# Kernel optimization log

Measured on AMD Instinct MI355X. Metric: run time of the kernel, lower is better.

The kernel has to match this reference:

```python
import jax, jax.numpy as jnp
import numpy as np

D_MODEL, H, D_FF = 1024, 16, 4096
B, S = 2, 2048
EPS = 1e-05


def layer_norm(x, gamma, beta):
    # Matches torch: mean and UNBIASED std over last dim, scalar gamma/beta,
    # and eps added to std (not variance).
    mean = jnp.mean(x, axis=-1, keepdims=True)
    var = jnp.sum((x - mean) ** 2, axis=-1, keepdims=True) / (x.shape[-1] - 1)
    return gamma * (x - mean) / (jnp.sqrt(var) + EPS) + beta


def setup_inputs() -> dict:
    key = jax.random.key(0)
    ks = jax.random.split(key, 16)
    sd = 1.0 / np.sqrt(D_MODEL)
    sf = 1.0 / np.sqrt(D_FF)
    return {
        "x": jax.random.normal(ks[0], (B, S, D_MODEL), jnp.float32),
        "mask": jnp.ones((1, 1, S, S), jnp.int32),
        "wq": jax.random.uniform(ks[1], (D_MODEL, D_MODEL), jnp.float32, -sd, sd),
        "bq": jax.random.uniform(ks[2], (D_MODEL,), jnp.float32, -sd, sd),
        "wk": jax.random.uniform(ks[3], (D_MODEL, D_MODEL), jnp.float32, -sd, sd),
        "bk": jax.random.uniform(ks[4], (D_MODEL,), jnp.float32, -sd, sd),
        "wv": jax.random.uniform(ks[5], (D_MODEL, D_MODEL), jnp.float32, -sd, sd),
        "bv": jax.random.uniform(ks[6], (D_MODEL,), jnp.float32, -sd, sd),
        "wo": jax.random.uniform(ks[7], (D_MODEL, D_MODEL), jnp.float32, -sd, sd),
        "bo": jax.random.uniform(ks[8], (D_MODEL,), jnp.float32, -sd, sd),
        "w1": jax.random.uniform(ks[9], (D_FF, D_MODEL), jnp.float32, -sd, sd),
        "b1": jax.random.uniform(ks[10], (D_FF,), jnp.float32, -sd, sd),
        "w2": jax.random.uniform(ks[11], (D_MODEL, D_FF), jnp.float32, -sf, sf),
        "b2": jax.random.uniform(ks[12], (D_MODEL,), jnp.float32, -sf, sf),
        "gamma1": jnp.ones((1,), jnp.float32),
        "beta1": jnp.zeros((1,), jnp.float32),
        "gamma2": jnp.ones((1,), jnp.float32),
        "beta2": jnp.zeros((1,), jnp.float32),
    }


def reference(x, mask, wq, bq, wk, bk, wv, bv, wo, bo, w1, b1, w2, b2,
              gamma1, beta1, gamma2, beta2):
    d_k = D_MODEL // H

    # --- residual 1: pre-LN self-attention ---
    xn = layer_norm(x, gamma1, beta1)
    q = (xn @ wq.T + bq).reshape(B, S, H, d_k).transpose(0, 2, 1, 3)
    k = (xn @ wk.T + bk).reshape(B, S, H, d_k).transpose(0, 2, 1, 3)
    v = (xn @ wv.T + bv).reshape(B, S, H, d_k).transpose(0, 2, 1, 3)

    scores = jnp.einsum("bhqd,bhkd->bhqk", q, k) / jnp.sqrt(
        jnp.asarray(d_k, x.dtype))
    scores = jnp.where(mask == 0, jnp.asarray(-1e9, x.dtype), scores)
    attn = jax.nn.softmax(scores, axis=-1)
    ctx = jnp.einsum("bhqk,bhkd->bhqd", attn, v)
    ctx = ctx.transpose(0, 2, 1, 3).reshape(B, S, D_MODEL)
    x = x + (ctx @ wo.T + bo)

    # --- residual 2: pre-LN feed-forward ---
    xn = layer_norm(x, gamma2, beta2)
    h = jax.nn.relu(xn @ w1.T + b1)
    x = x + (h @ w2.T + b2)
    return x
```

## Files before the change

kernel.cpp:

```cpp
#include <hip/hip_runtime.h>


typedef __bf16 bf16_t;
typedef __attribute__((ext_vector_type(8))) __bf16 bf16x8;
typedef __attribute__((ext_vector_type(4))) __bf16 bf16x4;
typedef __attribute__((ext_vector_type(4))) float f32x4;

#define MB (1024ull * 1024ull)
#define QSCALE 0.18033688011112043f

__device__ __forceinline__ void gload_lds16(const bf16_t* g, bf16_t* l) {
    __builtin_amdgcn_global_load_lds(
        (const __attribute__((address_space(1))) void*)g,
        (__attribute__((address_space(3))) void*)l, 16, 0, 0);
}

__device__ __forceinline__ int swz(int row, int col) {
    return row * 64 + ((((col >> 3) ^ row) & 7) << 3) + (col & 7);
}

__global__ __launch_bounds__(256) void cvt_kernel(const float* __restrict__ in,
                                                  bf16_t* __restrict__ out, int n4) {
    int i = blockIdx.x * 256 + threadIdx.x;
    if (i < n4) {
        float4 v = ((const float4*)in)[i];
        bf16x4 o = {(__bf16)v.x, (__bf16)v.y, (__bf16)v.z, (__bf16)v.w};
        ((bf16x4*)out)[i] = o;
    }
}

__global__ __launch_bounds__(256) void ln_kernel(const float* __restrict__ x,
                                                 bf16_t* __restrict__ out,
                                                 const float* __restrict__ gamma,
                                                 const float* __restrict__ beta) {
    const int lane = threadIdx.x & 63;
    const int row = blockIdx.x * 4 + (threadIdx.x >> 6);
    const float* xr = x + (size_t)row * 1024;
    float4 v[4];
    float s = 0.f;
#pragma unroll
    for (int i = 0; i < 4; ++i) {
        v[i] = ((const float4*)xr)[i * 64 + lane];
        s += v[i].x + v[i].y + v[i].z + v[i].w;
    }
#pragma unroll
    for (int o = 32; o; o >>= 1) s += __shfl_xor(s, o);
    float mean = s * (1.f / 1024.f);
    float vs = 0.f;
#pragma unroll
    for (int i = 0; i < 4; ++i) {
        float a = v[i].x - mean, b = v[i].y - mean, c = v[i].z - mean, d = v[i].w - mean;
        vs += a * a + b * b + c * c + d * d;
    }
#pragma unroll
    for (int o = 32; o; o >>= 1) vs += __shfl_xor(vs, o);
    float inv = 1.f / (sqrtf(vs * (1.f / 1023.f)) + 1e-5f);
    float g = gamma[0] * inv, bb = beta[0];
    bf16_t* orow = out + (size_t)row * 1024;
#pragma unroll
    for (int i = 0; i < 4; ++i) {
        bf16x4 ov = {(__bf16)((v[i].x - mean) * g + bb), (__bf16)((v[i].y - mean) * g + bb),
                     (__bf16)((v[i].z - mean) * g + bb), (__bf16)((v[i].w - mean) * g + bb)};
        *(bf16x4*)(orow + (i * 64 + lane) * 4) = ov;
    }
}

template <int KERN>
__global__ __launch_bounds__(512, 2) void gemm256(
    const bf16_t* __restrict__ A, const bf16_t* __restrict__ Bw, int K,
    const float* __restrict__ bias0, const float* __restrict__ bias1,
    const float* __restrict__ bias2, void* __restrict__ o0, void* __restrict__ o1,
    void* __restrict__ o2) {
    __shared__ bf16_t L[4 * 16384];
    const int t = threadIdx.x, lane = t & 63, w = t >> 6;
    const int wm = w >> 2, wn = w & 3;
    const int l15 = lane & 15, l4 = lane >> 4;
    const int bm = blockIdx.x, bn = blockIdx.y;
    const int NT = K >> 5;
    const bf16_t* Ab = A + (size_t)bm * 256 * K;
    const bf16_t* Bb = Bw + (size_t)bn * 256 * K;
    const int srow = t >> 2, pcol = (t & 3) * 8;
    f32x4 acc[8][4] = {};

    auto stageA = [&](int tt) {
        bf16_t* s = L + (tt & 3) * 16384;
        const int kb = tt * 32;
#pragma unroll
        for (int i = 0; i < 2; ++i) {
            int row = i * 128 + srow;
            int lcol = pcol ^ ((row & 3) << 3);
            gload_lds16(Ab + (size_t)row * K + kb + lcol, s + i * 4096 + t * 8);
        }
    };
    auto stageB = [&](int tt) {
        bf16_t* s = L + (tt & 3) * 16384 + 8192;
        const int kb = tt * 32;
#pragma unroll
        for (int i = 0; i < 2; ++i) {
            int row = i * 128 + srow;
            int lcol = pcol ^ ((row & 3) << 3);
            gload_lds16(Bb + (size_t)row * K + kb + lcol, s + i * 4096 + t * 8);
        }
    };

    stageA(0); stageB(0); stageA(1); stageB(1); stageA(2); stageB(2);
    asm volatile("s_waitcnt vmcnt(8)" ::: "memory");
    __builtin_amdgcn_s_barrier();

    for (int tt = 0; tt < NT; ++tt) {
        bf16_t* s = L + (tt & 3) * 16384;
        bf16_t* sB = s + 8192;
        bf16x8 af[4], bfr[4];
#pragma unroll
        for (int m = 0; m < 4; ++m) {
            int row = wm * 128 + m * 16 + l15;
            af[m] = *(const bf16x8*)(s + row * 32 + ((l4 * 8) ^ ((row & 3) << 3)));
        }
#pragma unroll
        for (int n = 0; n < 4; ++n) {
            int row = wn * 64 + n * 16 + l15;
            bfr[n] = *(const bf16x8*)(sB + row * 32 + ((l4 * 8) ^ ((row & 3) << 3)));
        }
        if (tt + 3 < NT) stageA(tt + 3);
        __builtin_amdgcn_s_barrier();
        __builtin_amdgcn_s_setprio(1);
#pragma unroll
        for (int m = 0; m < 4; ++m)
#pragma unroll
            for (int n = 0; n < 4; ++n)
                acc[m][n] = __builtin_amdgcn_mfma_f32_16x16x32_bf16(af[m], bfr[n], acc[m][n],
                                                                   0, 0, 0);
        __builtin_amdgcn_s_setprio(0);
        __builtin_amdgcn_s_barrier();
#pragma unroll
        for (int m = 0; m < 4; ++m) {
            int row = wm * 128 + 64 + m * 16 + l15;
            af[m] = *(const bf16x8*)(s + row * 32 + ((l4 * 8) ^ ((row & 3) << 3)));
        }
        if (tt + 3 < NT) stageB(tt + 3);
        __builtin_amdgcn_s_barrier();
        __builtin_amdgcn_s_setprio(1);
#pragma unroll
        for (int m = 0; m < 4; ++m)
#pragma unroll
            for (int n = 0; n < 4; ++n)
                acc[4 + m][n] = __builtin_amdgcn_mfma_f32_16x16x32_bf16(af[m], bfr[n],
                                                                       acc[4 + m][n], 0, 0, 0);
        __builtin_amdgcn_s_setprio(0);
        if (tt + 3 < NT)
            asm volatile("s_waitcnt vmcnt(8)" ::: "memory");
        else if (tt + 2 < NT)
            asm volatile("s_waitcnt vmcnt(4)" ::: "memory");
        else
            asm volatile("s_waitcnt vmcnt(0)" ::: "memory");
        __builtin_amdgcn_s_barrier();
    }

    if (KERN == 1) {
        const int colb = bn * 256 + wn * 64;
        float bb[4];
#pragma unroll
        for (int n = 0; n < 4; ++n) bb[n] = bias0[colb + n * 16 + l15];
#pragma unroll
        for (int m = 0; m < 8; ++m) {
            const int row0 = bm * 256 + wm * 128 + m * 16 + (l4 << 2);
#pragma unroll
            for (int n = 0; n < 4; ++n)
#pragma unroll
                for (int j = 0; j < 4; ++j) {
                    float v = acc[m][n][j] + bb[n];
                    ((bf16_t*)o0)[(size_t)(row0 + j) * 4096 + colb + n * 16 + l15] =
                        (bf16_t)(v > 0.f ? v : 0.f);
                }
        }
        return;
    }
    if (bn < 8) {
        const bool isq = bn < 4;
        const float* bias = isq ? bias0 : bias1;
        const int head = (bn & 3) * 4 + wn;
        const int b = (bm * 256) >> 11;
        const int srow0 = (bm * 256 + wm * 128) & 2047;
        bf16_t* dst = (bf16_t*)(isq ? o0 : o1) + ((size_t)(b * 16 + head) << 17);
        float bb[4];
#pragma unroll
        for (int n = 0; n < 4; ++n) bb[n] = bias[head * 64 + n * 16 + l15];
#pragma unroll
        for (int m = 0; m < 8; ++m)
#pragma unroll
            for (int n = 0; n < 4; ++n)
#pragma unroll
                for (int j = 0; j < 4; ++j) {
                    int srw = srow0 + m * 16 + (l4 << 2) + j;
                    float v = acc[m][n][j] + bb[n];
                    if (isq) v *= QSCALE;
                    dst[((size_t)srw << 6) + n * 16 + l15] = (bf16_t)v;
                }
    } else {
        const int head = (bn - 8) * 4 + wn;
        const int b = (bm * 256) >> 11;
        const int sbase = (bm * 256 + wm * 128) & 2047;
        bf16_t* P = L + w * 8192;
        float bb[4];
#pragma unroll
        for (int n = 0; n < 4; ++n) bb[n] = bias2[head * 64 + n * 16 + l15];
#pragma unroll
        for (int m = 0; m < 8; ++m)
#pragma unroll
            for (int n = 0; n < 4; ++n) {
                int d = n * 16 + l15;
                int sl = m * 16 + (l4 << 2);
                bf16x4 pk = {(__bf16)(acc[m][n][0] + bb[n]), (__bf16)(acc[m][n][1] + bb[n]),
                             (__bf16)(acc[m][n][2] + bb[n]), (__bf16)(acc[m][n][3] + bb[n])};
                *(bf16x4*)(P + d * 128 + (sl ^ ((d & 7) << 3))) = pk;
            }
#pragma unroll
        for (int p = 0; p < 16; ++p) {
            int id = p * 64 + lane;
            int d = id >> 4, c8 = (id & 15) * 8;
            bf16x8 vv = *(const bf16x8*)(P + d * 128 + (c8 ^ ((d & 7) << 3)));
            *(bf16x8*)((bf16_t*)o2 + (((size_t)(b * 16 + head) * 64 + d) << 11) + sbase + c8) =
                vv;
        }
    }
}

__global__ __launch_bounds__(256, 2) void gemm128p(
    const bf16_t* __restrict__ A, const bf16_t* __restrict__ Bw, int K,
    const float* __restrict__ bias, const float* __restrict__ resid,
    float* __restrict__ out) {
    __shared__ bf16_t L[4 * 6144];
    const int t = threadIdx.x, lane = t & 63, w = t >> 6;
    const int wr = w >> 1, wc = w & 1;
    const int l15 = lane & 15, l4 = lane >> 4;
    const int bm = blockIdx.x, bn = blockIdx.y;
    const int NT = K >> 5;
    const bf16_t* Ab = A + (size_t)bm * 64 * K;
    const bf16_t* Bb = Bw + (size_t)bn * 128 * K;
    const int srow = t >> 2, pcol = (t & 3) * 8;
    f32x4 acc[2][4] = {};

    auto STAGE = [&](int tt) {
        bf16_t* s = L + (tt & 3) * 6144;
        const int kb = tt * 32;
        {
            int lcol = pcol ^ ((srow & 3) << 3);
            gload_lds16(Ab + (size_t)srow * K + kb + lcol, s + t * 8);
        }
#pragma unroll
        for (int i = 0; i < 2; ++i) {
            int row = i * 64 + srow;
            int lcol = pcol ^ ((row & 3) << 3);
            gload_lds16(Bb + (size_t)row * K + kb + lcol, s + 2048 + i * 2048 + t * 8);
        }
    };

    STAGE(0); STAGE(1); STAGE(2);
    asm volatile("s_waitcnt vmcnt(6)" ::: "memory");
    __builtin_amdgcn_s_barrier();

    for (int tt = 0; tt < NT; ++tt) {
        bf16_t* s = L + (tt & 3) * 6144;
        bf16x8 af[2], bfr[4];
#pragma unroll
        for (int m = 0; m < 2; ++m) {
            int row = wr * 32 + m * 16 + l15;
            af[m] = *(const bf16x8*)(s + row * 32 + ((l4 * 8) ^ ((row & 3) << 3)));
        }
#pragma unroll
        for (int n = 0; n < 4; ++n) {
            int row = wc * 64 + n * 16 + l15;
            bfr[n] = *(const bf16x8*)(s + 2048 + row * 32 + ((l4 * 8) ^ ((row & 3) << 3)));
        }
        if (tt + 3 < NT) STAGE(tt + 3);
        __builtin_amdgcn_s_barrier();
        __builtin_amdgcn_s_setprio(1);
#pragma unroll
        for (int m = 0; m < 2; ++m)
#pragma unroll
            for (int n = 0; n < 4; ++n)
                acc[m][n] = __builtin_amdgcn_mfma_f32_16x16x32_bf16(af[m], bfr[n], acc[m][n],
                                                                   0, 0, 0);
        __builtin_amdgcn_s_setprio(0);
        if (tt + 3 < NT)
            asm volatile("s_waitcnt vmcnt(6)" ::: "memory");
        else if (tt + 2 < NT)
            asm volatile("s_waitcnt vmcnt(3)" ::: "memory");
        else
            asm volatile("s_waitcnt vmcnt(0)" ::: "memory");
        __builtin_amdgcn_s_barrier();
    }

#pragma unroll
    for (int m = 0; m < 2; ++m) {
        const int row0 = bm * 64 + wr * 32 + m * 16 + (l4 << 2);
#pragma unroll
        for (int n = 0; n < 4; ++n) {
            const int col = bn * 128 + wc * 64 + n * 16 + l15;
#pragma unroll
            for (int j = 0; j < 4; ++j) {
                const int row = row0 + j;
                out[(size_t)row * 1024 + col] =
                    resid[(size_t)row * 1024 + col] + acc[m][n][j] + bias[col];
            }
        }
    }
}

__global__ __launch_bounds__(256) void attn_kernel(const bf16_t* __restrict__ q,
                                                   const bf16_t* __restrict__ k,
                                                   const bf16_t* __restrict__ vt,
                                                   bf16_t* __restrict__ ctx) {
    __shared__ bf16_t Kl[64 * 64];
    __shared__ bf16_t Vl[64 * 64];
    __shared__ bf16_t Pl[4][16 * 64];
    const int t = threadIdx.x, lane = t & 63, w = t >> 6;
    const int qt0 = blockIdx.x * 64;
    const int bh = blockIdx.y;
    const bf16_t* qg = q + (size_t)bh * 2048 * 64;
    const bf16_t* kg = k + (size_t)bh * 2048 * 64;
    const bf16_t* vg = vt + (size_t)bh * 64 * 2048;
    const int r = t >> 3, c8 = (t & 7) * 8;
    const int l15 = lane & 15, l4 = lane >> 4;

    *(bf16x8*)(Kl + swz(r, c8)) = *(const bf16x8*)(qg + (size_t)(qt0 + r) * 64 + c8);
    *(bf16x8*)(Kl + swz(r + 32, c8)) = *(const bf16x8*)(qg + (size_t)(qt0 + r + 32) * 64 + c8);
    __syncthreads();
    bf16x8 qf[2];
    qf[0] = *(const bf16x8*)(Kl + swz(w * 16 + l15, l4 * 8));
    qf[1] = *(const bf16x8*)(Kl + swz(w * 16 + l15, 32 + l4 * 8));
    __syncthreads();

    f32x4 o[4] = {};
    float mi = -1e30f, li = 0.f;

    {
        bf16x8 k0 = *(const bf16x8*)(kg + (size_t)r * 64 + c8);
        bf16x8 k1 = *(const bf16x8*)(kg + (size_t)(r + 32) * 64 + c8);
        bf16x8 v0 = *(const bf16x8*)(vg + (size_t)r * 2048 + c8);
        bf16x8 v1 = *(const bf16x8*)(vg + (size_t)(r + 32) * 2048 + c8);
        *(bf16x8*)(Kl + swz(r, c8)) = k0;
        *(bf16x8*)(Kl + swz(r + 32, c8)) = k1;
        *(bf16x8*)(Vl + swz(r, c8)) = v0;
        *(bf16x8*)(Vl + swz(r + 32, c8)) = v1;
    }

    for (int kt = 0; kt < 2048; kt += 64) {
        __syncthreads();
        bf16x8 k0, k1, v0, v1;
        const bool more = (kt + 64) < 2048;
        if (more) {
            k0 = *(const bf16x8*)(kg + (size_t)(kt + 64 + r) * 64 + c8);
            k1 = *(const bf16x8*)(kg + (size_t)(kt + 64 + r + 32) * 64 + c8);
            v0 = *(const bf16x8*)(vg + (size_t)r * 2048 + kt + 64 + c8);
            v1 = *(const bf16x8*)(vg + (size_t)(r + 32) * 2048 + kt + 64 + c8);
        }
        f32x4 sT[4] = {};
        __builtin_amdgcn_s_setprio(1);
#pragma unroll
        for (int kk = 0; kk < 2; ++kk) {
            bf16x8 kf[4];
#pragma unroll
            for (int n = 0; n < 4; ++n)
                kf[n] = *(const bf16x8*)(Kl + swz(n * 16 + l15, kk * 32 + l4 * 8));
#pragma unroll
            for (int n = 0; n < 4; ++n)
                sT[n] = __builtin_amdgcn_mfma_f32_16x16x32_bf16(kf[n], qf[kk], sT[n], 0, 0, 0);
        }
        __builtin_amdgcn_s_setprio(0);
        float mx = fmaxf(fmaxf(sT[0][0], sT[0][1]), fmaxf(sT[0][2], sT[0][3]));
#pragma unroll
        for (int n = 1; n < 4; ++n)
            mx = fmaxf(mx, fmaxf(fmaxf(sT[n][0], sT[n][1]), fmaxf(sT[n][2], sT[n][3])));
        mx = fmaxf(mx, __shfl_xor(mx, 16));
        mx = fmaxf(mx, __shfl_xor(mx, 32));
        if (!__all(mx <= mi + 8.f)) {
            float mn = fmaxf(mi, mx);
            float al = exp2f(mi - mn);
            mi = mn;
            li *= al;
#pragma unroll
            for (int jr = 0; jr < 4; ++jr) {
                float alo = __shfl(al, (lane & 0x30) | (l4 * 4 + jr));
#pragma unroll
                for (int n = 0; n < 4; ++n) o[n][jr] *= alo;
            }
        }
        float rs = 0.f;
#pragma unroll
        for (int n = 0; n < 4; ++n) {
            float p0 = exp2f(sT[n][0] - mi);
            float p1 = exp2f(sT[n][1] - mi);
            float p2 = exp2f(sT[n][2] - mi);
            float p3 = exp2f(sT[n][3] - mi);
            rs += (p0 + p1) + (p2 + p3);
            bf16x4 pk = {(__bf16)p0, (__bf16)p1, (__bf16)p2, (__bf16)p3};
            *(bf16x4*)(&Pl[w][swz(l15, n * 16 + (l4 << 2))]) = pk;
        }
        rs += __shfl_xor(rs, 16);
        rs += __shfl_xor(rs, 32);
        li += rs;
        __builtin_amdgcn_s_setprio(1);
#pragma unroll
        for (int kk = 0; kk < 2; ++kk) {
            bf16x8 pa = *(const bf16x8*)(&Pl[w][swz(l15, kk * 32 + l4 * 8)]);
            bf16x8 vb[4];
#pragma unroll
            for (int n = 0; n < 4; ++n)
                vb[n] = *(const bf16x8*)(Vl + swz(n * 16 + l15, kk * 32 + l4 * 8));
#pragma unroll
            for (int n = 0; n < 4; ++n)
                o[n] = __builtin_amdgcn_mfma_f32_16x16x32_bf16(pa, vb[n], o[n], 0, 0, 0);
        }
        __builtin_amdgcn_s_setprio(0);
        __syncthreads();
        if (more) {
            *(bf16x8*)(Kl + swz(r, c8)) = k0;
            *(bf16x8*)(Kl + swz(r + 32, c8)) = k1;
            *(bf16x8*)(Vl + swz(r, c8)) = v0;
            *(bf16x8*)(Vl + swz(r + 32, c8)) = v1;
        }
    }
#pragma unroll
    for (int jr = 0; jr < 4; ++jr) {
        float inv = 1.f / __shfl(li, (lane & 0x30) | (l4 * 4 + jr));
        int row = qt0 + w * 16 + l4 * 4 + jr;
        size_t base = ((size_t)(bh >> 4) * 2048 + row) * 1024 + (bh & 15) * 64;
#pragma unroll
        for (int n = 0; n < 4; ++n)
            ctx[base + n * 16 + l15] = (bf16_t)(o[n][jr] * inv);
    }
}

extern "C" void kernel_launch(void* const* d_in, const int* in_sizes, int n_in,
                              void* d_out, int out_size, void* d_ws, size_t ws_size,
                              hipStream_t stream) {
    const float* x = (const float*)d_in[0];
    const float* wq = (const float*)d_in[2];
    const float* bq = (const float*)d_in[3];
    const float* wk = (const float*)d_in[4];
    const float* bk = (const float*)d_in[5];
    const float* wv = (const float*)d_in[6];
    const float* bv = (const float*)d_in[7];
    const float* wo = (const float*)d_in[8];
    const float* bo = (const float*)d_in[9];
    const float* w1 = (const float*)d_in[10];
    const float* b1 = (const float*)d_in[11];
    const float* w2 = (const float*)d_in[12];
    const float* b2 = (const float*)d_in[13];
    const float* gamma1 = (const float*)d_in[14];
    const float* beta1 = (const float*)d_in[15];
    const float* gamma2 = (const float*)d_in[16];
    const float* beta2 = (const float*)d_in[17];

    char* ws = (char*)d_ws;
    bf16_t* wqkv = (bf16_t*)(ws + 0);
    bf16_t* wob = (bf16_t*)(ws + 6 * MB);
    bf16_t* w1b = (bf16_t*)(ws + 8 * MB);
    bf16_t* w2b = (bf16_t*)(ws + 16 * MB);
    bf16_t* xnb = (bf16_t*)(ws + 24 * MB);
    bf16_t* qb = (bf16_t*)(ws + 32 * MB);
    bf16_t* kb = (bf16_t*)(ws + 40 * MB);
    bf16_t* vtb = (bf16_t*)(ws + 48 * MB);
    bf16_t* ctxb = (bf16_t*)(ws + 56 * MB);
    float* x1 = (float*)(ws + 64 * MB);
    bf16_t* hb = (bf16_t*)(ws + 32 * MB);

    cvt_kernel<<<1024, 256, 0, stream>>>(wq, wqkv, 262144);
    cvt_kernel<<<1024, 256, 0, stream>>>(wk, wqkv + 1024 * 1024, 262144);
    cvt_kernel<<<1024, 256, 0, stream>>>(wv, wqkv + 2 * 1024 * 1024, 262144);
    cvt_kernel<<<1024, 256, 0, stream>>>(wo, wob, 262144);
    cvt_kernel<<<4096, 256, 0, stream>>>(w1, w1b, 1048576);
    cvt_kernel<<<4096, 256, 0, stream>>>(w2, w2b, 1048576);

    ln_kernel<<<1024, 256, 0, stream>>>(x, xnb, gamma1, beta1);
    gemm256<0><<<dim3(16, 12), 512, 0, stream>>>(xnb, wqkv, 1024, bq, bk, bv, qb, kb, vtb);
    attn_kernel<<<dim3(32, 32), 256, 0, stream>>>(qb, kb, vtb, ctxb);
    gemm128p<<<dim3(64, 8), 256, 0, stream>>>(ctxb, wob, 1024, bo, x, x1);
    ln_kernel<<<1024, 256, 0, stream>>>(x1, xnb, gamma2, beta2);
    gemm256<1><<<dim3(16, 16), 512, 0, stream>>>(xnb, w1b, 1024, b1, nullptr, nullptr, hb,
                                                 nullptr, nullptr);
    gemm128p<<<dim3(64, 8), 256, 0, stream>>>(hb, w2b, 4096, b2, x1, (float*)d_out);
}
```

Baseline: 260.0 us.

## Rewrite attention with 32x32x16 MFMA and register-resident P via permlane swap

The attention kernel now gives each wave 32 query rows and uses 32x32x16 bf16 MFMAs. Q fragments load straight from global memory, and the softmax probabilities are repacked in registers with permlane32_swap instead of a round-trip through LDS. This halves the grid, doubles K/V reuse per block, drops the per-row alpha shuffles and uses the hardware exp2. The six weight-conversion launches are merged into a single kernel to cut launch overhead. The trade-off is higher register pressure (launch_bounds 256,2) and fewer blocks for the attention grid.

```diff
diff --git a/kernel.cpp b/kernel.cpp
--- a/kernel.cpp
+++ b/kernel.cpp
@@ -4,7 +4,11 @@
 typedef __bf16 bf16_t;
 typedef __attribute__((ext_vector_type(8))) __bf16 bf16x8;
 typedef __attribute__((ext_vector_type(4))) __bf16 bf16x4;
+typedef __attribute__((ext_vector_type(2))) __bf16 bf16x2;
 typedef __attribute__((ext_vector_type(4))) float f32x4;
+typedef __attribute__((ext_vector_type(16))) float f32x16;
+typedef __attribute__((ext_vector_type(2))) unsigned uint32x2;
+typedef __attribute__((ext_vector_type(4))) unsigned uint32x4;
 
 #define MB (1024ull * 1024ull)
 #define QSCALE 0.18033688011112043f
@@ -19,14 +23,30 @@
     return row * 64 + ((((col >> 3) ^ row) & 7) << 3) + (col & 7);
 }
 
-__global__ __launch_bounds__(256) void cvt_kernel(const float* __restrict__ in,
-                                                  bf16_t* __restrict__ out, int n4) {
-    int i = blockIdx.x * 256 + threadIdx.x;
-    if (i < n4) {
-        float4 v = ((const float4*)in)[i];
-        bf16x4 o = {(__bf16)v.x, (__bf16)v.y, (__bf16)v.z, (__bf16)v.w};
-        ((bf16x4*)out)[i] = o;
-    }
+__device__ __forceinline__ unsigned cvtpk(float a, float b) {
+    bf16x2 v = {(__bf16)a, (__bf16)b};
+    return __builtin_bit_cast(unsigned, v);
+}
+
+__global__ __launch_bounds__(256) void cvt_all(
+    const float* __restrict__ wq, const float* __restrict__ wk,
+    const float* __restrict__ wv, const float* __restrict__ wo,
+    const float* __restrict__ w1, const float* __restrict__ w2,
+    bf16_t* __restrict__ wqkv, bf16_t* __restrict__ wob, bf16_t* __restrict__ w1b,
+    bf16_t* __restrict__ w2b) {
+    const int b = blockIdx.x, t = threadIdx.x;
+    const float* in;
+    bf16_t* out;
+    int i;
+    if (b < 1024) { in = wq; out = wqkv; i = b * 256 + t; }
+    else if (b < 2048) { in = wk; out = wqkv + 1048576; i = (b - 1024) * 256 + t; }
+    else if (b < 3072) { in = wv; out = wqkv + 2097152; i = (b - 2048) * 256 + t; }
+    else if (b < 4096) { in = wo; out = wob; i = (b - 3072) * 256 + t; }
+    else if (b < 8192) { in = w1; out = w1b; i = (b - 4096) * 256 + t; }
+    else { in = w2; out = w2b; i = (b - 8192) * 256 + t; }
+    float4 v = ((const float4*)in)[i];
+    bf16x4 o = {(__bf16)v.x, (__bf16)v.y, (__bf16)v.z, (__bf16)v.w};
+    ((bf16x4*)out)[i] = o;
 }
 
 __global__ __launch_bounds__(256) void ln_kernel(const float* __restrict__ x,
@@ -307,31 +327,27 @@
     }
 }
 
-__global__ __launch_bounds__(256) void attn_kernel(const bf16_t* __restrict__ q,
-                                                   const bf16_t* __restrict__ k,
-                                                   const bf16_t* __restrict__ vt,
-                                                   bf16_t* __restrict__ ctx) {
+__global__ __launch_bounds__(256, 2) void attn_kernel(const bf16_t* __restrict__ q,
+                                                      const bf16_t* __restrict__ k,
+                                                      const bf16_t* __restrict__ vt,
+                                                      bf16_t* __restrict__ ctx) {
     __shared__ bf16_t Kl[64 * 64];
     __shared__ bf16_t Vl[64 * 64];
-    __shared__ bf16_t Pl[4][16 * 64];
     const int t = threadIdx.x, lane = t & 63, w = t >> 6;
-    const int qt0 = blockIdx.x * 64;
     const int bh = blockIdx.y;
     const bf16_t* qg = q + (size_t)bh * 2048 * 64;
     const bf16_t* kg = k + (size_t)bh * 2048 * 64;
     const bf16_t* vg = vt + (size_t)bh * 64 * 2048;
     const int r = t >> 3, c8 = (t & 7) * 8;
-    const int l15 = lane & 15, l4 = lane >> 4;
-
-    *(bf16x8*)(Kl + swz(r, c8)) = *(const bf16x8*)(qg + (size_t)(qt0 + r) * 64 + c8);
-    *(bf16x8*)(Kl + swz(r + 32, c8)) = *(const bf16x8*)(qg + (size_t)(qt0 + r + 32) * 64 + c8);
-    __syncthreads();
-    bf16x8 qf[2];
-    qf[0] = *(const bf16x8*)(Kl + swz(w * 16 + l15, l4 * 8));
-    qf[1] = *(const bf16x8*)(Kl + swz(w * 16 + l15, 32 + l4 * 8));
-    __syncthreads();
-
-    f32x4 o[4] = {};
+    const int l31 = lane & 31, h = lane >> 5;
+    const int qrow = blockIdx.x * 128 + w * 32 + l31;
+
+    bf16x8 qf[4];
+#pragma unroll
+    for (int kd = 0; kd < 4; ++kd)
+        qf[kd] = *(const bf16x8*)(qg + (size_t)qrow * 64 + kd * 16 + h * 8);
+
+    f32x16 o0 = {}, o1 = {};
     float mi = -1e30f, li = 0.f;
 
     {
@@ -355,62 +371,66 @@
             v0 = *(const bf16x8*)(vg + (size_t)r * 2048 + kt + 64 + c8);
             v1 = *(const bf16x8*)(vg + (size_t)(r + 32) * 2048 + kt + 64 + c8);
         }
-        f32x4 sT[4] = {};
+        f32x16 sT0 = {}, sT1 = {};
         __builtin_amdgcn_s_setprio(1);
 #pragma unroll
-        for (int kk = 0; kk < 2; ++kk) {
-            bf16x8 kf[4];
-#pragma unroll
-            for (int n = 0; n < 4; ++n)
-                kf[n] = *(const bf16x8*)(Kl + swz(n * 16 + l15, kk * 32 + l4 * 8));
-#pragma unroll
-            for (int n = 0; n < 4; ++n)
-                sT[n] = __builtin_amdgcn_mfma_f32_16x16x32_bf16(kf[n], qf[kk], sT[n], 0, 0, 0);
+        for (int kd = 0; kd < 4; ++kd) {
+            bf16x8 ka0 = *(const bf16x8*)(Kl + swz(l31, kd * 16 + h * 8));
+            bf16x8 ka1 = *(const bf16x8*)(Kl + swz(32 + l31, kd * 16 + h * 8));
+            sT0 = __builtin_amdgcn_mfma_f32_32x32x16_bf16(ka0, qf[kd], sT0, 0, 0, 0);
+            sT1 = __builtin_amdgcn_mfma_f32_32x32x16_bf16(ka1, qf[kd], sT1, 0, 0, 0);
         }
         __builtin_amdgcn_s_setprio(0);
-        float mx = fmaxf(fmaxf(sT[0][0], sT[0][1]), fmaxf(sT[0][2], sT[0][3]));
-#pragma unroll
-        for (int n = 1; n < 4; ++n)
-            mx = fmaxf(mx, fmaxf(fmaxf(sT[n][0], sT[n][1]), fmaxf(sT[n][2], sT[n][3])));
-        mx = fmaxf(mx, __shfl_xor(mx, 16));
+        float mx = fmaxf(sT0[0], sT0[1]);
+#pragma unroll
+        for (int i = 2; i < 16; ++i) mx = fmaxf(mx, sT0[i]);
+#pragma unroll
+        for (int i = 0; i < 16; ++i) mx = fmaxf(mx, sT1[i]);
         mx = fmaxf(mx, __shfl_xor(mx, 32));
         if (!__all(mx <= mi + 8.f)) {
             float mn = fmaxf(mi, mx);
-            float al = exp2f(mi - mn);
+            float al = __builtin_amdgcn_exp2f(mi - mn);
             mi = mn;
             li *= al;
-#pragma unroll
-            for (int jr = 0; jr < 4; ++jr) {
-                float alo = __shfl(al, (lane & 0x30) | (l4 * 4 + jr));
-#pragma unroll
-                for (int n = 0; n < 4; ++n) o[n][jr] *= alo;
-            }
-        }
+            o0 *= al;
+            o1 *= al;
+        }
+        f32x16 e0, e1;
         float rs = 0.f;
 #pragma unroll
-        for (int n = 0; n < 4; ++n) {
-            float p0 = exp2f(sT[n][0] - mi);
-            float p1 = exp2f(sT[n][1] - mi);
-            float p2 = exp2f(sT[n][2] - mi);
-            float p3 = exp2f(sT[n][3] - mi);
-            rs += (p0 + p1) + (p2 + p3);
-            bf16x4 pk = {(__bf16)p0, (__bf16)p1, (__bf16)p2, (__bf16)p3};
-            *(bf16x4*)(&Pl[w][swz(l15, n * 16 + (l4 << 2))]) = pk;
-        }
-        rs += __shfl_xor(rs, 16);
+        for (int i = 0; i < 16; ++i) {
+            e0[i] = __builtin_amdgcn_exp2f(sT0[i] - mi);
+            rs += e0[i];
+        }
+#pragma unroll
+        for (int i = 0; i < 16; ++i) {
+            e1[i] = __builtin_amdgcn_exp2f(sT1[i] - mi);
+            rs += e1[i];
+        }
         rs += __shfl_xor(rs, 32);
         li += rs;
+        bf16x8 pa[4];
+#pragma unroll
+        for (int kd = 0; kd < 4; ++kd) {
+            const f32x16& e = (kd < 2) ? e0 : e1;
+            const int R0l = 8 * (kd & 1);
+            const int R0h = R0l + 4;
+            unsigned U0 = cvtpk(e[R0l + 0], e[R0l + 1]);
+            unsigned V0 = cvtpk(e[R0l + 2], e[R0l + 3]);
+            unsigned U1 = cvtpk(e[R0h + 0], e[R0h + 1]);
+            unsigned V1 = cvtpk(e[R0h + 2], e[R0h + 3]);
+            uint32x2 ru = __builtin_amdgcn_permlane32_swap(U0, U1, false, false);
+            uint32x2 rv = __builtin_amdgcn_permlane32_swap(V0, V1, false, false);
+            uint32x4 pw = {ru.x, rv.x, ru.y, rv.y};
+            pa[kd] = __builtin_bit_cast(bf16x8, pw);
+        }
         __builtin_amdgcn_s_setprio(1);
 #pragma unroll
-        for (int kk = 0; kk < 2; ++kk) {
-            bf16x8 pa = *(const bf16x8*)(&Pl[w][swz(l15, kk * 32 + l4 * 8)]);
-            bf16x8 vb[4];
-#pragma unroll
-            for (int n = 0; n < 4; ++n)
-                vb[n] = *(const bf16x8*)(Vl + swz(n * 16 + l15, kk * 32 + l4 * 8));
-#pragma unroll
-            for (int n = 0; n < 4; ++n)
-                o[n] = __builtin_amdgcn_mfma_f32_16x16x32_bf16(pa, vb[n], o[n], 0, 0, 0);
+        for (int kd = 0; kd < 4; ++kd) {
+            bf16x8 va0 = *(const bf16x8*)(Vl + swz(l31, kd * 16 + h * 8));
+            bf16x8 va1 = *(const bf16x8*)(Vl + swz(32 + l31, kd * 16 + h * 8));
+            o0 = __builtin_amdgcn_mfma_f32_32x32x16_bf16(va0, pa[kd], o0, 0, 0, 0);
+            o1 = __builtin_amdgcn_mfma_f32_32x32x16_bf16(va1, pa[kd], o1, 0, 0, 0);
         }
         __builtin_amdgcn_s_setprio(0);
         __syncthreads();
@@ -421,14 +441,16 @@
             *(bf16x8*)(Vl + swz(r + 32, c8)) = v1;
         }
     }
-#pragma unroll
-    for (int jr = 0; jr < 4; ++jr) {
-        float inv = 1.f / __shfl(li, (lane & 0x30) | (l4 * 4 + jr));
-        int row = qt0 + w * 16 + l4 * 4 + jr;
-        size_t base = ((size_t)(bh >> 4) * 2048 + row) * 1024 + (bh & 15) * 64;
-#pragma unroll
-        for (int n = 0; n < 4; ++n)
-            ctx[base + n * 16 + l15] = (bf16_t)(o[n][jr] * inv);
+    float inv = 1.f / li;
+    size_t base = ((size_t)(bh >> 4) * 2048 + qrow) * 1024 + (bh & 15) * 64;
+#pragma unroll
+    for (int g = 0; g < 4; ++g) {
+        bf16x4 ov0 = {(__bf16)(o0[4 * g + 0] * inv), (__bf16)(o0[4 * g + 1] * inv),
+                      (__bf16)(o0[4 * g + 2] * inv), (__bf16)(o0[4 * g + 3] * inv)};
+        *(bf16x4*)(ctx + base + 8 * g + 4 * h) = ov0;
+        bf16x4 ov1 = {(__bf16)(o1[4 * g + 0] * inv), (__bf16)(o1[4 * g + 1] * inv),
+                      (__bf16)(o1[4 * g + 2] * inv), (__bf16)(o1[4 * g + 3] * inv)};
+        *(bf16x4*)(ctx + base + 32 + 8 * g + 4 * h) = ov1;
     }
 }
 
@@ -466,16 +488,11 @@
     float* x1 = (float*)(ws + 64 * MB);
     bf16_t* hb = (bf16_t*)(ws + 32 * MB);
 
-    cvt_kernel<<<1024, 256, 0, stream>>>(wq, wqkv, 262144);
-    cvt_kernel<<<1024, 256, 0, stream>>>(wk, wqkv + 1024 * 1024, 262144);
-    cvt_kernel<<<1024, 256, 0, stream>>>(wv, wqkv + 2 * 1024 * 1024, 262144);
-    cvt_kernel<<<1024, 256, 0, stream>>>(wo, wob, 262144);
-    cvt_kernel<<<4096, 256, 0, stream>>>(w1, w1b, 1048576);
-    cvt_kernel<<<4096, 256, 0, stream>>>(w2, w2b, 1048576);
+    cvt_all<<<12288, 256, 0, stream>>>(wq, wk, wv, wo, w1, w2, wqkv, wob, w1b, w2b);
 
     ln_kernel<<<1024, 256, 0, stream>>>(x, xnb, gamma1, beta1);
     gemm256<0><<<dim3(16, 12), 512, 0, stream>>>(xnb, wqkv, 1024, bq, bk, bv, qb, kb, vtb);
-    attn_kernel<<<dim3(32, 32), 256, 0, stream>>>(qb, kb, vtb, ctxb);
+    attn_kernel<<<dim3(16, 32), 256, 0, stream>>>(qb, kb, vtb, ctxb);
     gemm128p<<<dim3(64, 8), 256, 0, stream>>>(ctxb, wob, 1024, bo, x, x1);
     ln_kernel<<<1024, 256, 0, stream>>>(x1, xnb, gamma2, beta2);
     gemm256<1><<<dim3(16, 16), 512, 0, stream>>>(xnb, w1b, 1024, b1, nullptr, nullptr, hb,
```

Measured after the change: 227.7 us. 12.4% less time.
